# Optimization experiments

Measured on AMD Instinct MI355X. Metric: run time of the kernel, lower is better.

Reference implementation:

```python
import jax, jax.numpy as jnp
import numpy as np

B, S, HID = 4, 2048, 512
NH, HD = 8, 64          # num heads, head dim (num_kv_heads == NH, so GQA group = 1)
SW = 250                # sliding window
THETA = 10000.0
SCALING = 1.0 / np.sqrt(HD)
NEG_INF = jnp.finfo(jnp.float32).min


def setup_inputs() -> dict:
    key = jax.random.key(0)
    ks = jax.random.split(key, 5)
    w_std = 1.0 / np.sqrt(HID)
    return {
        "hidden_states": jax.random.normal(ks[0], (B, S, HID), jnp.float32),
        "position_ids": jnp.broadcast_to(jnp.arange(S, dtype=jnp.int64), (B, S)),
        "Wq": jax.random.normal(ks[1], (NH * HD, HID), jnp.float32) * w_std,
        "Wk": jax.random.normal(ks[2], (NH * HD, HID), jnp.float32) * w_std,
        "Wv": jax.random.normal(ks[3], (NH * HD, HID), jnp.float32) * w_std,
        "Wo": jax.random.normal(ks[4], (HID, NH * HD), jnp.float32) * w_std,
    }


def _rotate_half(x):
    x1, x2 = jnp.split(x, 2, axis=-1)
    return jnp.concatenate((-x2, x1), axis=-1)


def reference(hidden_states, position_ids, Wq, Wk, Wv, Wo):
    b, s, _ = hidden_states.shape
    dtype = hidden_states.dtype

    # QKV projections (Linear: x @ W.T, no bias) -> [b, h, s, d]
    q = (hidden_states @ Wq.T).reshape(b, s, NH, HD).transpose(0, 2, 1, 3)
    k = (hidden_states @ Wk.T).reshape(b, s, NH, HD).transpose(0, 2, 1, 3)
    v = (hidden_states @ Wv.T).reshape(b, s, NH, HD).transpose(0, 2, 1, 3)

    # Rotary embedding (MimiRotaryEmbedding), computed in fp32
    inv_freq = 1.0 / (THETA ** (jnp.arange(0, HD, 2, dtype=jnp.float32) / HD))
    freqs = position_ids.astype(jnp.float32)[:, :, None] * inv_freq[None, None, :]  # [b, s, HD/2]
    emb = jnp.concatenate((freqs, freqs), axis=-1)                                   # [b, s, HD]
    cos = jnp.cos(emb).astype(dtype)[:, None, :, :]  # unsqueeze head dim
    sin = jnp.sin(emb).astype(dtype)[:, None, :, :]
    q = q * cos + _rotate_half(q) * sin
    k = k * cos + _rotate_half(k) * sin

    # Sliding-window causal additive mask: keep kv iff q_idx >= kv_idx and q_idx - kv_idx <= SW
    idx = jnp.arange(s)
    keep = (idx[:, None] >= idx[None, :]) & ((idx[:, None] - idx[None, :]) <= SW)
    bias = jnp.where(keep, 0.0, NEG_INF).astype(jnp.float32)  # [s, s]

    # Eager attention: full scores, fp32 softmax (num_key_value_groups == 1)
    scores = jnp.einsum("bhqd,bhkd->bhqk", q, k) * SCALING
    scores = scores.astype(jnp.float32) + bias[None, None, :, :]
    attn = jax.nn.softmax(scores, axis=-1).astype(dtype)
    out = jnp.einsum("bhqk,bhkd->bhqd", attn, v)

    # merge heads and output projection
    out = out.transpose(0, 2, 1, 3).reshape(b, s, NH * HD)
    return out @ Wo.T
```

## Files before the change

### kernel.cpp

```cpp
#include <hip/hip_runtime.h>
#include <hip/hip_bf16.h>
#include <math.h>


#define B_   4
#define S_   2048
#define HID_ 512
#define NH_  8
#define HD_  64
#define SW_  250

typedef __bf16 bf16x8 __attribute__((ext_vector_type(8)));
typedef __bf16 bf16x4 __attribute__((ext_vector_type(4)));
typedef float f32x4 __attribute__((ext_vector_type(4)));
using bf16_t = __hip_bfloat16;
typedef unsigned int u32;

__device__ __forceinline__ void glds16(const void* g, void* l) {
    __builtin_amdgcn_global_load_lds(
        (const __attribute__((address_space(1))) u32*)g,
        (__attribute__((address_space(3))) u32*)l, 16, 0, 0);
}

__global__ __launch_bounds__(256) void cvt_all(
    const float* __restrict__ X,  const float* __restrict__ Wq,
    const float* __restrict__ Wk, const float* __restrict__ Wv,
    const float* __restrict__ Wo,
    bf16_t* __restrict__ Xb, bf16_t* __restrict__ Wcat, bf16_t* __restrict__ Wob)
{
    const int blk = blockIdx.x;
    const float* s; bf16_t* d; size_t base;
    if (blk < 2048)      { s = X;  d = Xb;            base = (size_t)blk * 2048; }
    else if (blk < 2176) { s = Wq; d = Wcat;          base = (size_t)(blk - 2048) * 2048; }
    else if (blk < 2304) { s = Wk; d = Wcat + 262144; base = (size_t)(blk - 2176) * 2048; }
    else if (blk < 2432) { s = Wv; d = Wcat + 524288; base = (size_t)(blk - 2304) * 2048; }
    else                 { s = Wo; d = Wob;           base = (size_t)(blk - 2432) * 2048; }
    size_t i = base + (size_t)threadIdx.x * 8;
    float4 a = *reinterpret_cast<const float4*>(s + i);
    float4 b = *reinterpret_cast<const float4*>(s + i + 4);
    bf16x8 r;
    r[0] = (__bf16)a.x; r[1] = (__bf16)a.y; r[2] = (__bf16)a.z; r[3] = (__bf16)a.w;
    r[4] = (__bf16)b.x; r[5] = (__bf16)b.y; r[6] = (__bf16)b.z; r[7] = (__bf16)b.w;
    *reinterpret_cast<bf16x8*>(d + i) = r;
}

__global__ __launch_bounds__(256) void qkv_gemm(
    const bf16_t* __restrict__ Xb, const bf16_t* __restrict__ Wcat,
    bf16_t* __restrict__ Q, bf16_t* __restrict__ Kbuf, bf16_t* __restrict__ Vt)
{
    __shared__ __align__(16) char smem_raw[34816];
    bf16_t* const sm = (bf16_t*)smem_raw;
    const int tid = threadIdx.x;
    const int wave = tid >> 6, lane = tid & 63;
    const int quad = lane >> 4, l16 = lane & 15;
    const int wm = wave & 1, wn = wave >> 1;

    const int g = blockIdx.x;
    const int xcd = g & 7, slot = g >> 3;
    const int mi = xcd * 8 + (slot & 7);
    const int ni = slot >> 3;
    const int m0 = mi * 128, n0 = ni * 128;

    const int srow0 = tid >> 2,           sl0 = (tid & 3) ^ ((srow0 >> 1) & 3);
    const int srow1 = (256 + tid) >> 2,   sl1 = ((256 + tid) & 3) ^ ((srow1 >> 1) & 3);

    glds16(Xb   + (size_t)(m0 + srow0) * HID_ + sl0 * 8, sm + tid * 8);
    glds16(Wcat + (size_t)(n0 + srow0) * HID_ + sl0 * 8, sm + 4096 + tid * 8);
    glds16(Xb   + (size_t)(m0 + srow1) * HID_ + sl1 * 8, sm + (256 + tid) * 8);
    glds16(Wcat + (size_t)(n0 + srow1) * HID_ + sl1 * 8, sm + 4096 + (256 + tid) * 8);

    f32x4 acc[4][4] = {};
    for (int t = 0; t < 16; ++t) {
        const int curo = (t & 1) * 8192;
        if (t + 1 < 16) {
            const int nxto = curo ^ 8192;
            const int k1 = (t + 1) * 32;
            glds16(Xb   + (size_t)(m0 + srow0) * HID_ + k1 + sl0 * 8, sm + nxto + tid * 8);
            glds16(Wcat + (size_t)(n0 + srow0) * HID_ + k1 + sl0 * 8, sm + nxto + 4096 + tid * 8);
            glds16(Xb   + (size_t)(m0 + srow1) * HID_ + k1 + sl1 * 8, sm + nxto + (256 + tid) * 8);
            glds16(Wcat + (size_t)(n0 + srow1) * HID_ + k1 + sl1 * 8, sm + nxto + 4096 + (256 + tid) * 8);
            asm volatile("s_waitcnt vmcnt(4)" ::: "memory");
        } else {
            asm volatile("s_waitcnt vmcnt(0)" ::: "memory");
        }
        __builtin_amdgcn_sched_barrier(0);
        __builtin_amdgcn_s_barrier();
        __builtin_amdgcn_sched_barrier(0);
        asm volatile("" ::: "memory");

        bf16x8 af[4], bfr[4];
#pragma unroll
        for (int i = 0; i < 4; ++i) {
            int ra = wm * 64 + i * 16 + l16;
            int rb = wn * 64 + i * 16 + l16;
            int pa = quad ^ ((ra >> 1) & 3);
            int pb = quad ^ ((rb >> 1) & 3);
            af[i]  = *reinterpret_cast<const bf16x8*>(sm + curo + ra * 32 + pa * 8);
            bfr[i] = *reinterpret_cast<const bf16x8*>(sm + curo + 4096 + rb * 32 + pb * 8);
        }
#pragma unroll
        for (int mi2 = 0; mi2 < 4; ++mi2)
#pragma unroll
            for (int ni2 = 0; ni2 < 4; ++ni2)
                acc[mi2][ni2] = __builtin_amdgcn_mfma_f32_16x16x32_bf16(af[mi2], bfr[ni2], acc[mi2][ni2], 0, 0, 0);
        asm volatile("" ::: "memory");
        __builtin_amdgcn_sched_barrier(0);
        __builtin_amdgcn_s_barrier();
        __builtin_amdgcn_sched_barrier(0);
        asm volatile("" ::: "memory");
    }

    const int seg = n0 >> 9;
    const int hh = ((n0 & 511) + wn * 64) >> 6;
    bf16_t* wt = sm + wave * 4352;
    const int mbase = m0 + wm * 64;
    const int bb = mbase >> 11;
    const int sbase = mbase & (S_ - 1);

    if (seg < 2) {
        const float qs = (seg == 0) ? 0.125f : 1.0f;
        const float c = 0.41524101186f;
        float inv0 = exp2f(-(float)l16 * c);
        float inv1 = exp2f(-(float)(l16 + 16) * c);
#pragma unroll
        for (int mi2 = 0; mi2 < 4; ++mi2)
#pragma unroll
            for (int r = 0; r < 4; ++r) {
                int lrow = mi2 * 16 + quad * 4 + r;
                float sf = (float)(sbase + lrow);
#pragma unroll
                for (int ip = 0; ip < 2; ++ip) {
                    float sn, cs_;
                    __sincosf(sf * (ip ? inv1 : inv0), &sn, &cs_);
                    float x1 = acc[mi2][ip][r], x2 = acc[mi2][ip + 2][r];
                    wt[lrow * 68 + ip * 16 + l16]      = __float2bfloat16((x1 * cs_ - x2 * sn) * qs);
                    wt[lrow * 68 + ip * 16 + l16 + 32] = __float2bfloat16((x2 * cs_ + x1 * sn) * qs);
                }
            }
        bf16_t* Y = (seg == 0) ? Q : Kbuf;
#pragma unroll
        for (int it = 0; it < 8; ++it) {
            int e = it * 64 + lane;
            int sr = e >> 3, doff = (e & 7) * 8;
            size_t g2 = ((size_t)(bb * NH_ + hh) * S_ + sbase + sr) * HD_ + doff;
            *reinterpret_cast<bf16x8*>(Y + g2) =
                *reinterpret_cast<const bf16x8*>(wt + sr * 68 + doff);
        }
    } else {
#pragma unroll
        for (int mi2 = 0; mi2 < 4; ++mi2)
#pragma unroll
            for (int ni2 = 0; ni2 < 4; ++ni2)
#pragma unroll
                for (int r = 0; r < 4; ++r)
                    wt[(ni2 * 16 + l16) * 68 + mi2 * 16 + quad * 4 + r] =
                        __float2bfloat16(acc[mi2][ni2][r]);
#pragma unroll
        for (int it = 0; it < 8; ++it) {
            int e = it * 64 + lane;
            int d = e >> 3, soff = (e & 7) * 8;
            size_t g2 = ((size_t)(bb * NH_ + hh) * HD_ + d) * S_ + sbase + soff;
            *reinterpret_cast<bf16x8*>(Vt + g2) =
                *reinterpret_cast<const bf16x8*>(wt + d * 68 + soff);
        }
    }
}

__global__ __launch_bounds__(256) void attn_mfma(
    const bf16_t* __restrict__ Q, const bf16_t* __restrict__ K,
    const bf16_t* __restrict__ Vt, bf16_t* __restrict__ A)
{
    __shared__ __align__(16) __bf16 Ks[2][32 * 64];
    __shared__ __align__(16) __bf16 Vs[2][64 * 32];
    __shared__ __align__(16) __bf16 pt[4][16][40];
    __shared__ float sums_l[4][16];
    const int tid = threadIdx.x;
    const int wave = tid >> 6, lane = tid & 63;
    const int quad = lane >> 4, l16 = lane & 15;

    const int g = blockIdx.x;
    const int xcd = g & 7, slot = g >> 3;
    const int bh = xcd * 4 + (slot >> 5);
    const int qt = slot & 31;
    const int b = bh >> 3, h = bh & 7;
    const int q0b = qt * 64;
    const int q0 = q0b + wave * 16;

    const size_t bh_  = (size_t)(b * NH_ + h) * S_;
    const size_t bhd = (size_t)(b * NH_ + h) * HD_;

    bf16x8 qf0, qf1;
    {
        const bf16_t* qp = Q + (bh_ + q0 + l16) * HD_ + quad * 8;
        qf0 = *reinterpret_cast<const bf16x8*>(qp);
        qf1 = *reinterpret_cast<const bf16x8*>(qp + 32);
    }
    const int kstartB = (q0b > SW_) ? ((q0b - SW_) & ~31) : 0;
    const int ntB = (q0b + 95 - kstartB) >> 5;
    const int qq = q0 + l16;

    const int krow = tid >> 3, kl = (tid & 7) ^ (krow & 7);
    const int vrow = tid >> 2, vl = (tid & 3) ^ (vrow & 3);

    {
        const int kb = kstartB;
        glds16(K  + (bh_ + kb + krow) * HD_ + kl * 8, &Ks[0][tid * 8]);
        glds16(Vt + (bhd + vrow) * S_ + kb + vl * 8, &Vs[0][tid * 8]);
    }

    float sum = 0.f;
    f32x4 o[4] = {};
    for (int t = 0; t < ntB; ++t) {
        const int cur = t & 1;
        const int kb = kstartB + t * 32;
        if (t + 1 < ntB) {
            const int kb2 = kb + 32;
            glds16(K  + (bh_ + kb2 + krow) * HD_ + kl * 8, &Ks[cur ^ 1][tid * 8]);
            glds16(Vt + (bhd + vrow) * S_ + kb2 + vl * 8, &Vs[cur ^ 1][tid * 8]);
            asm volatile("s_waitcnt vmcnt(2)" ::: "memory");
        } else {
            asm volatile("s_waitcnt vmcnt(0)" ::: "memory");
        }
        __builtin_amdgcn_s_barrier();
        asm volatile("" ::: "memory");

#pragma unroll
        for (int half = 0; half < 2; ++half) {
            const int rowt = half * 16 + l16;
            const int p0 = quad ^ (rowt & 7);
            const int p1 = (quad ^ 4) ^ (rowt & 7);
            bf16x8 k0 = *reinterpret_cast<const bf16x8*>(&Ks[cur][rowt * 64 + p0 * 8]);
            bf16x8 k1 = *reinterpret_cast<const bf16x8*>(&Ks[cur][rowt * 64 + p1 * 8]);
            f32x4 z = {};
            z = __builtin_amdgcn_mfma_f32_16x16x32_bf16(k0, qf0, z, 0, 0, 0);
            z = __builtin_amdgcn_mfma_f32_16x16x32_bf16(k1, qf1, z, 0, 0, 0);
            const int kbase = kb + half * 16 + quad * 4;
            bf16x4 pk;
#pragma unroll
            for (int r = 0; r < 4; ++r) {
                int key = kbase + r;
                bool keep = (key <= qq) && (qq - key <= SW_);
                float p = keep ? __expf(z[r]) : 0.f;
                sum += p;
                pk[r] = (__bf16)p;
            }
            *reinterpret_cast<bf16x4*>(&pt[wave][l16][half * 16 + quad * 4]) = pk;
        }
        bf16x8 pf = *reinterpret_cast<const bf16x8*>(&pt[wave][l16][quad * 8]);
#pragma unroll
        for (int nf = 0; nf < 4; ++nf) {
            const int rowv = nf * 16 + l16;
            const int pv = quad ^ (rowv & 3);
            bf16x8 vf = *reinterpret_cast<const bf16x8*>(&Vs[cur][rowv * 32 + pv * 8]);
            o[nf] = __builtin_amdgcn_mfma_f32_16x16x32_bf16(pf, vf, o[nf], 0, 0, 0);
        }
        asm volatile("" ::: "memory");
        __builtin_amdgcn_s_barrier();
        asm volatile("" ::: "memory");
    }

    sum += __shfl_xor(sum, 16, 64);
    sum += __shfl_xor(sum, 32, 64);
    if (quad == 0) sums_l[wave][l16] = sum;
    float inv_l[4];
#pragma unroll
    for (int r = 0; r < 4; ++r) inv_l[r] = 1.0f / sums_l[wave][quad * 4 + r];
#pragma unroll
    for (int nf = 0; nf < 4; ++nf)
#pragma unroll
        for (int r = 0; r < 4; ++r) {
            int qr = q0 + quad * 4 + r;
            A[((size_t)(b * S_ + qr)) * HID_ + h * HD_ + nf * 16 + l16] =
                __float2bfloat16(o[nf][r] * inv_l[r]);
        }
}

__global__ __launch_bounds__(256) void out_proj(
    const bf16_t* __restrict__ Ain, const bf16_t* __restrict__ Wob,
    float* __restrict__ out)
{
    __shared__ __align__(16) bf16_t As[128 * 32];
    __shared__ __align__(16) bf16_t Bs[64 * 32];
    const int tid = threadIdx.x;
    const int wave = tid >> 6, lane = tid & 63;
    const int quad = lane >> 4, l16 = lane & 15;
    const int m0 = blockIdx.x * 128, n0 = blockIdx.y * 64;

    f32x4 acc[2][4] = {};
    for (int k0 = 0; k0 < HID_; k0 += 32) {
#pragma unroll
        for (int rr = 0; rr < 2; ++rr) {
            int slot = rr * 256 + tid;
            int row = slot >> 2;
            int l = (slot & 3) ^ ((row >> 1) & 3);
            glds16(Ain + (size_t)(m0 + row) * HID_ + k0 + l * 8, As + slot * 8);
        }
        {
            int slot = tid;
            int row = slot >> 2;
            int l = (slot & 3) ^ ((row >> 1) & 3);
            glds16(Wob + (size_t)(n0 + row) * HID_ + k0 + l * 8, Bs + slot * 8);
        }
        __syncthreads();
        bf16x8 af[2], bfr[4];
#pragma unroll
        for (int i = 0; i < 2; ++i) {
            int ra = wave * 32 + i * 16 + l16;
            int pa = quad ^ ((ra >> 1) & 3);
            af[i] = *reinterpret_cast<const bf16x8*>(&As[ra * 32 + pa * 8]);
        }
#pragma unroll
        for (int i = 0; i < 4; ++i) {
            int rb = i * 16 + l16;
            int pb = quad ^ ((rb >> 1) & 3);
            bfr[i] = *reinterpret_cast<const bf16x8*>(&Bs[rb * 32 + pb * 8]);
        }
#pragma unroll
        for (int mi = 0; mi < 2; ++mi)
#pragma unroll
            for (int ni = 0; ni < 4; ++ni)
                acc[mi][ni] = __builtin_amdgcn_mfma_f32_16x16x32_bf16(af[mi], bfr[ni], acc[mi][ni], 0, 0, 0);
        __syncthreads();
    }
#pragma unroll
    for (int mi = 0; mi < 2; ++mi)
#pragma unroll
        for (int ni = 0; ni < 4; ++ni)
#pragma unroll
            for (int r = 0; r < 4; ++r) {
                int m = m0 + wave * 32 + mi * 16 + quad * 4 + r;
                int n = n0 + ni * 16 + l16;
                out[(size_t)m * HID_ + n] = acc[mi][ni][r];
            }
}

extern "C" void kernel_launch(void* const* d_in, const int* in_sizes, int n_in,
                              void* d_out, int out_size, void* d_ws, size_t ws_size,
                              hipStream_t stream)
{
    const float* X  = (const float*)d_in[0];
    const float* Wq = (const float*)d_in[2];
    const float* Wk = (const float*)d_in[3];
    const float* Wv = (const float*)d_in[4];
    const float* Wo = (const float*)d_in[5];

    char* ws = (char*)d_ws;
    const size_t elems = (size_t)B_ * NH_ * S_ * HD_;
    const size_t wsz   = (size_t)HID_ * HID_;
    bf16_t* Q    = (bf16_t*)ws;
    bf16_t* K    = Q + elems;
    bf16_t* Vt   = K + elems;
    bf16_t* Xb   = Vt + elems;
    bf16_t* A    = Xb;
    bf16_t* Wcat = Xb + elems;
    bf16_t* Wob  = Wcat + 3 * wsz;

    cvt_all<<<2560, 256, 0, stream>>>(X, Wq, Wk, Wv, Wo, Xb, Wcat, Wob);
    qkv_gemm<<<768, 256, 0, stream>>>(Xb, Wcat, Q, K, Vt);
    attn_mfma<<<1024, 256, 0, stream>>>(Q, K, Vt, A);
    out_proj<<<dim3(64, 8), 256, 0, stream>>>(A, Wob, (float*)d_out);
}
```

Baseline: 125.6 us.

## Process two query sub-tiles per wave in attention to reuse K/V tiles

New measurement: 128.7 us. 2.5% more time.

```diff
diff --git a/kernel.cpp b/kernel.cpp
--- a/kernel.cpp
+++ b/kernel.cpp
@@ -86,7 +86,6 @@
         __builtin_amdgcn_sched_barrier(0);
         __builtin_amdgcn_s_barrier();
         __builtin_amdgcn_sched_barrier(0);
-        asm volatile("" ::: "memory");
 
         bf16x8 af[4], bfr[4];
 #pragma unroll
@@ -107,7 +106,6 @@
         __builtin_amdgcn_sched_barrier(0);
         __builtin_amdgcn_s_barrier();
         __builtin_amdgcn_sched_barrier(0);
-        asm volatile("" ::: "memory");
     }
 
     const int seg = n0 >> 9;
@@ -172,32 +170,36 @@
 {
     __shared__ __align__(16) __bf16 Ks[2][32 * 64];
     __shared__ __align__(16) __bf16 Vs[2][64 * 32];
-    __shared__ __align__(16) __bf16 pt[4][16][40];
-    __shared__ float sums_l[4][16];
+    __shared__ __align__(16) __bf16 pt[4][2][16][40];
+    __shared__ float sums_l[4][2][16];
     const int tid = threadIdx.x;
     const int wave = tid >> 6, lane = tid & 63;
     const int quad = lane >> 4, l16 = lane & 15;
 
     const int g = blockIdx.x;
     const int xcd = g & 7, slot = g >> 3;
-    const int bh = xcd * 4 + (slot >> 5);
-    const int qt = slot & 31;
+    const int bh = xcd * 4 + (slot >> 4);
+    const int qt = slot & 15;
     const int b = bh >> 3, h = bh & 7;
-    const int q0b = qt * 64;
-    const int q0 = q0b + wave * 16;
-
-    const size_t bh_  = (size_t)(b * NH_ + h) * S_;
+    const int q0b = qt * 128;
+    const int q0A = q0b + wave * 16;
+    const int q0B = q0A + 64;
+
+    const size_t bh_ = (size_t)(b * NH_ + h) * S_;
     const size_t bhd = (size_t)(b * NH_ + h) * HD_;
 
-    bf16x8 qf0, qf1;
+    bf16x8 qfA0, qfA1, qfB0, qfB1;
     {
-        const bf16_t* qp = Q + (bh_ + q0 + l16) * HD_ + quad * 8;
-        qf0 = *reinterpret_cast<const bf16x8*>(qp);
-        qf1 = *reinterpret_cast<const bf16x8*>(qp + 32);
+        const bf16_t* qp = Q + (bh_ + q0A + l16) * HD_ + quad * 8;
+        qfA0 = *reinterpret_cast<const bf16x8*>(qp);
+        qfA1 = *reinterpret_cast<const bf16x8*>(qp + 32);
+        const bf16_t* qp2 = Q + (bh_ + q0B + l16) * HD_ + quad * 8;
+        qfB0 = *reinterpret_cast<const bf16x8*>(qp2);
+        qfB1 = *reinterpret_cast<const bf16x8*>(qp2 + 32);
     }
     const int kstartB = (q0b > SW_) ? ((q0b - SW_) & ~31) : 0;
-    const int ntB = (q0b + 95 - kstartB) >> 5;
-    const int qq = q0 + l16;
+    const int ntB = (q0b + 159 - kstartB) >> 5;
+    const int qqA = q0A + l16, qqB = q0B + l16;
 
     const int krow = tid >> 3, kl = (tid & 7) ^ (krow & 7);
     const int vrow = tid >> 2, vl = (tid & 3) ^ (vrow & 3);
@@ -208,8 +210,8 @@
         glds16(Vt + (bhd + vrow) * S_ + kb + vl * 8, &Vs[0][tid * 8]);
     }
 
-    float sum = 0.f;
-    f32x4 o[4] = {};
+    float sumA = 0.f, sumB = 0.f;
+    f32x4 oA[4] = {}, oB[4] = {};
     for (int t = 0; t < ntB; ++t) {
         const int cur = t & 1;
         const int kb = kstartB + t * 32;
@@ -231,47 +233,62 @@
             const int p1 = (quad ^ 4) ^ (rowt & 7);
             bf16x8 k0 = *reinterpret_cast<const bf16x8*>(&Ks[cur][rowt * 64 + p0 * 8]);
             bf16x8 k1 = *reinterpret_cast<const bf16x8*>(&Ks[cur][rowt * 64 + p1 * 8]);
-            f32x4 z = {};
-            z = __builtin_amdgcn_mfma_f32_16x16x32_bf16(k0, qf0, z, 0, 0, 0);
-            z = __builtin_amdgcn_mfma_f32_16x16x32_bf16(k1, qf1, z, 0, 0, 0);
+            f32x4 zA = {}, zB = {};
+            zA = __builtin_amdgcn_mfma_f32_16x16x32_bf16(k0, qfA0, zA, 0, 0, 0);
+            zA = __builtin_amdgcn_mfma_f32_16x16x32_bf16(k1, qfA1, zA, 0, 0, 0);
+            zB = __builtin_amdgcn_mfma_f32_16x16x32_bf16(k0, qfB0, zB, 0, 0, 0);
+            zB = __builtin_amdgcn_mfma_f32_16x16x32_bf16(k1, qfB1, zB, 0, 0, 0);
             const int kbase = kb + half * 16 + quad * 4;
-            bf16x4 pk;
+            bf16x4 pkA, pkB;
 #pragma unroll
             for (int r = 0; r < 4; ++r) {
                 int key = kbase + r;
-                bool keep = (key <= qq) && (qq - key <= SW_);
-                float p = keep ? __expf(z[r]) : 0.f;
-                sum += p;
-                pk[r] = (__bf16)p;
+                bool keepA = (key <= qqA) && (qqA - key <= SW_);
+                bool keepB = (key <= qqB) && (qqB - key <= SW_);
+                float pA = keepA ? __expf(zA[r]) : 0.f;
+                float pB = keepB ? __expf(zB[r]) : 0.f;
+                sumA += pA; sumB += pB;
+                pkA[r] = (__bf16)pA; pkB[r] = (__bf16)pB;
             }
-            *reinterpret_cast<bf16x4*>(&pt[wave][l16][half * 16 + quad * 4]) = pk;
-        }
-        bf16x8 pf = *reinterpret_cast<const bf16x8*>(&pt[wave][l16][quad * 8]);
+            *reinterpret_cast<bf16x4*>(&pt[wave][0][l16][half * 16 + quad * 4]) = pkA;
+            *reinterpret_cast<bf16x4*>(&pt[wave][1][l16][half * 16 + quad * 4]) = pkB;
+        }
+        bf16x8 pfA = *reinterpret_cast<const bf16x8*>(&pt[wave][0][l16][quad * 8]);
+        bf16x8 pfB = *reinterpret_cast<const bf16x8*>(&pt[wave][1][l16][quad * 8]);
 #pragma unroll
         for (int nf = 0; nf < 4; ++nf) {
             const int rowv = nf * 16 + l16;
             const int pv = quad ^ (rowv & 3);
             bf16x8 vf = *reinterpret_cast<const bf16x8*>(&Vs[cur][rowv * 32 + pv * 8]);
-            o[nf] = __builtin_amdgcn_mfma_f32_16x16x32_bf16(pf, vf, o[nf], 0, 0, 0);
+            oA[nf] = __builtin_amdgcn_mfma_f32_16x16x32_bf16(pfA, vf, oA[nf], 0, 0, 0);
+            oB[nf] = __builtin_amdgcn_mfma_f32_16x16x32_bf16(pfB, vf, oB[nf], 0, 0, 0);
         }
         asm volatile("" ::: "memory");
         __builtin_amdgcn_s_barrier();
         asm volatile("" ::: "memory");
     }
 
-    sum += __shfl_xor(sum, 16, 64);
-    sum += __shfl_xor(sum, 32, 64);
-    if (quad == 0) sums_l[wave][l16] = sum;
-    float inv_l[4];
-#pragma unroll
-    for (int r = 0; r < 4; ++r) inv_l[r] = 1.0f / sums_l[wave][quad * 4 + r];
+    sumA += __shfl_xor(sumA, 16, 64);
+    sumA += __shfl_xor(sumA, 32, 64);
+    sumB += __shfl_xor(sumB, 16, 64);
+    sumB += __shfl_xor(sumB, 32, 64);
+    if (quad == 0) { sums_l[wave][0][l16] = sumA; sums_l[wave][1][l16] = sumB; }
+    float invA[4], invB[4];
+#pragma unroll
+    for (int r = 0; r < 4; ++r) {
+        invA[r] = 1.0f / sums_l[wave][0][quad * 4 + r];
+        invB[r] = 1.0f / sums_l[wave][1][quad * 4 + r];
+    }
 #pragma unroll
     for (int nf = 0; nf < 4; ++nf)
 #pragma unroll
         for (int r = 0; r < 4; ++r) {
-            int qr = q0 + quad * 4 + r;
-            A[((size_t)(b * S_ + qr)) * HID_ + h * HD_ + nf * 16 + l16] =
-                __float2bfloat16(o[nf][r] * inv_l[r]);
+            int qrA = q0A + quad * 4 + r;
+            int qrB = q0B + quad * 4 + r;
+            A[((size_t)(b * S_ + qrA)) * HID_ + h * HD_ + nf * 16 + l16] =
+                __float2bfloat16(oA[nf][r] * invA[r]);
+            A[((size_t)(b * S_ + qrB)) * HID_ + h * HD_ + nf * 16 + l16] =
+                __float2bfloat16(oB[nf][r] * invB[r]);
         }
 }
 
@@ -357,6 +374,6 @@
 
     cvt_all<<<2560, 256, 0, stream>>>(X, Wq, Wk, Wv, Wo, Xb, Wcat, Wob);
     qkv_gemm<<<768, 256, 0, stream>>>(Xb, Wcat, Q, K, Vt);
-    attn_mfma<<<1024, 256, 0, stream>>>(Q, K, Vt, A);
+    attn_mfma<<<512, 256, 0, stream>>>(Q, K, Vt, A);
     out_proj<<<dim3(64, 8), 256, 0, stream>>>(A, Wob, (float*)d_out);
 }
```
